# Kernel optimization log

Measured on AMD Instinct MI355X. Metric: run time of the kernel, lower is better.

Reference implementation:

```python
import jax, jax.numpy as jnp
import numpy as np

D = 256      # d_model
NH = 8       # heads
HD = D // NH # head dim = 32
NL = 4       # feature levels
NP = 4       # sampling points per head per level
DFF = 1024   # ffn hidden
LAYERS = 6
SHAPES = [(48, 48), (24, 24), (12, 12), (6, 6)]


def setup_inputs() -> dict:
    key = jax.random.key(0)
    ks = jax.random.split(key, 20)
    bs = 2
    inp = {}
    for i, (h, w) in enumerate(SHAPES):
        inp[f"src{i}"] = jax.random.normal(ks[i], (bs, D, h, w), jnp.float32)
        inp[f"pos{i}"] = jax.random.normal(ks[4 + i], (bs, D, h, w), jnp.float32)

    def p(k, shape, s=0.02):
        return jax.random.normal(k, shape, jnp.float32) * s

    inp["level_embed"] = p(ks[8], (NL, D), 1.0)
    inp["Wv"] = p(ks[9], (LAYERS, D, D))
    inp["bv"] = jnp.zeros((LAYERS, D))
    inp["Woff"] = p(ks[10], (LAYERS, D, NH * NL * NP * 2), 0.001)
    inp["boff"] = p(ks[11], (LAYERS, NH * NL * NP * 2), 0.5)
    inp["Wa"] = p(ks[12], (LAYERS, D, NH * NL * NP))
    inp["ba"] = jnp.zeros((LAYERS, NH * NL * NP))
    inp["Wo"] = p(ks[13], (LAYERS, D, D))
    inp["bo"] = jnp.zeros((LAYERS, D))
    inp["g1"] = jnp.ones((LAYERS, D))
    inp["beta1"] = jnp.zeros((LAYERS, D))
    inp["W1"] = p(ks[14], (LAYERS, D, DFF))
    inp["bf1"] = jnp.zeros((LAYERS, DFF))
    inp["W2"] = p(ks[15], (LAYERS, DFF, D))
    inp["bf2"] = jnp.zeros((LAYERS, D))
    inp["g2"] = jnp.ones((LAYERS, D))
    inp["beta2"] = jnp.zeros((LAYERS, D))
    return inp


def _ln(x, g, b):
    m = x.mean(-1, keepdims=True)
    v = ((x - m) ** 2).mean(-1, keepdims=True)
    return (x - m) / jnp.sqrt(v + 1e-5) * g + b


def _bilinear(value, loc, H, W):
    # value: (bs, NH, H*W, HD); loc: (bs, Len, NH, NP, 2) in [0,1]
    # grid_sample, align_corners=False, zero padding
    bs, Len, nh, P, _ = loc.shape
    x = loc[..., 0] * W - 0.5
    y = loc[..., 1] * H - 0.5
    x0 = jnp.floor(x)
    y0 = jnp.floor(y)
    lx = x - x0
    ly = y - y0
    x0i = x0.astype(jnp.int32)
    y0i = y0.astype(jnp.int32)
    out = jnp.zeros((bs, nh, Len, P, value.shape[-1]), value.dtype)
    for dy, dx, w in ((0, 0, (1 - lx) * (1 - ly)), (0, 1, lx * (1 - ly)),
                      (1, 0, (1 - lx) * ly), (1, 1, lx * ly)):
        xi = x0i + dx
        yi = y0i + dy
        valid = (xi >= 0) & (xi < W) & (yi >= 0) & (yi < H)
        idx = jnp.clip(yi, 0, H - 1) * W + jnp.clip(xi, 0, W - 1)  # (bs,Len,NH,P)
        idx_t = idx.transpose(0, 2, 1, 3).reshape(bs, nh, Len * P)
        v = jnp.take_along_axis(value, idx_t[..., None], axis=2)
        v = v.reshape(bs, nh, Len, P, -1)
        wm = (w * valid).transpose(0, 2, 1, 3)  # (bs,NH,Len,P)
        out = out + v * wm[..., None]
    return out


def _msda(q, src, ref, shapes, starts, Wv, bv, Woff, boff, Wa, ba, Wo, bo):
    bs, Len, _ = q.shape
    value = (src @ Wv + bv).reshape(bs, Len, NH, HD)
    off = (q @ Woff + boff).reshape(bs, Len, NH, NL, NP, 2)
    attn = jax.nn.softmax((q @ Wa + ba).reshape(bs, Len, NH, NL * NP), -1)
    attn = attn.reshape(bs, Len, NH, NL, NP)
    acc = jnp.zeros((bs, NH, Len, HD), q.dtype)
    for lv, (H, W) in enumerate(shapes):
        norm = jnp.array([W, H], q.dtype)
        loc = ref[None, :, None, None, :] + off[:, :, :, lv] / norm  # (bs,Len,NH,NP,2)
        v = value[:, starts[lv]:starts[lv] + H * W].transpose(0, 2, 1, 3)
        samp = _bilinear(v, loc, H, W)  # (bs,NH,Len,NP,HD)
        acc = acc + (samp * attn[:, :, :, lv].transpose(0, 2, 1, 3)[..., None]).sum(3)
    return acc.transpose(0, 2, 1, 3).reshape(bs, Len, D) @ Wo + bo


def _encode(srcs, poss, level_embed, Wv, bv, Woff, boff, Wa, ba, Wo, bo,
            g1, beta1, W1, bf1, W2, bf2, g2, beta2):
    shapes = [(s.shape[2], s.shape[3]) for s in srcs]
    bs = srcs[0].shape[0]
    src_flat = jnp.concatenate(
        [s.reshape(bs, D, -1).transpose(0, 2, 1) for s in srcs], 1)
    pos_flat = jnp.concatenate(
        [p.reshape(bs, D, -1).transpose(0, 2, 1) + level_embed[i][None, None]
         for i, p in enumerate(poss)], 1)
    starts = np.cumsum([0] + [h * w for h, w in shapes])[:-1]
    # reference points (masks are all-zero so valid_ratios == 1)
    refs = []
    for (H, W) in shapes:
        ry, rx = jnp.meshgrid(jnp.linspace(0.5, H - 0.5, H) / H,
                              jnp.linspace(0.5, W - 0.5, W) / W, indexing='ij')
        refs.append(jnp.stack([rx.reshape(-1), ry.reshape(-1)], -1))
    ref = jnp.concatenate(refs, 0)  # (Len, 2)

    out = src_flat
    for l in range(LAYERS):
        q = out + pos_flat
        out2 = _msda(q, out, ref, shapes, starts, Wv[l], bv[l], Woff[l],
                     boff[l], Wa[l], ba[l], Wo[l], bo[l])
        out = _ln(out + out2, g1[l], beta1[l])
        h = jax.nn.relu(out @ W1[l] + bf1[l])
        out = _ln(out + h @ W2[l] + bf2[l], g2[l], beta2[l])
    return out, shapes, starts


def reference(src0, src1, src2, src3, pos0, pos1, pos2, pos3, level_embed,
              Wv, bv, Woff, boff, Wa, ba, Wo, bo,
              g1, beta1, W1, bf1, W2, bf2, g2, beta2):
    memory, shapes, starts = _encode(
        [src0, src1, src2, src3], [pos0, pos1, pos2, pos3], level_embed,
        Wv, bv, Woff, boff, Wa, ba, Wo, bo,
        g1, beta1, W1, bf1, W2, bf2, g2, beta2)
    spatial_shapes = jnp.array(shapes, jnp.int32)
    level_start_index = jnp.array(np.asarray(starts), jnp.int32)
    return memory, spatial_shapes, level_start_index
```

## Files before the change

kernel.cpp:

```cpp
#include <hip/hip_runtime.h>
#include <math.h>

#define D_MODEL 256
#define NHEAD 8
#define HDIM 32
#define NLVL 4
#define NPTS 4
#define DFF 1024
#define NLAYERS 6
#define LEN 3060
#define BS 2
#define MROWS (BS * LEN)
#define MPAD 6144

typedef __attribute__((ext_vector_type(8))) short bf16x8;
typedef __attribute__((ext_vector_type(4))) float f32x4;

__device__ __forceinline__ unsigned short f2bf(float f) {
    union { float f; unsigned u; } v; v.f = f;
    unsigned r = v.u + 0x7FFF + ((v.u >> 16) & 1);
    return (unsigned short)(r >> 16);
}

#define GLDS(gp, lp) __builtin_amdgcn_global_load_lds(                        \
    (const __attribute__((address_space(1))) void*)(gp),                      \
    (__attribute__((address_space(3))) void*)(lp), 16, 0, 0)

__global__ __launch_bounds__(256) void flatten_kernel(
    const float* __restrict__ s0, const float* __restrict__ s1,
    const float* __restrict__ s2, const float* __restrict__ s3,
    const float* __restrict__ p0, const float* __restrict__ p1,
    const float* __restrict__ p2, const float* __restrict__ p3,
    const float* __restrict__ lemb,
    float* __restrict__ out, unsigned short* __restrict__ outbf,
    float* __restrict__ pos)
{
    int gid = blockIdx.x * 256 + threadIdx.x;
    if (gid >= MROWS * D_MODEL) return;
    int d  = gid & (D_MODEL - 1);
    int bt = gid >> 8;
    int b  = (bt >= LEN) ? 1 : 0;
    int t  = bt - b * LEN;

    int lv, li, hw;
    const float* sp; const float* pp;
    if (t < 2304)      { lv = 0; li = t;        hw = 2304; sp = s0; pp = p0; }
    else if (t < 2880) { lv = 1; li = t - 2304; hw = 576;  sp = s1; pp = p1; }
    else if (t < 3024) { lv = 2; li = t - 2880; hw = 144;  sp = s2; pp = p2; }
    else               { lv = 3; li = t - 3024; hw = 36;   sp = s3; pp = p3; }

    size_t si = (size_t)(b * D_MODEL + d) * hw + li;
    float v = sp[si];
    out[gid]   = v;
    outbf[gid] = f2bf(v);
    pos[gid]   = pp[si] + lemb[lv * D_MODEL + d];
}

__global__ __launch_bounds__(256) void addq_kernel(
    const float4* __restrict__ a, const float4* __restrict__ b,
    ushort4* __restrict__ qbf, int n4)
{
    int i = blockIdx.x * 256 + threadIdx.x;
    if (i >= n4) return;
    float4 x = a[i], y = b[i];
    qbf[i] = make_ushort4(f2bf(x.x + y.x), f2bf(x.y + y.y),
                          f2bf(x.z + y.z), f2bf(x.w + y.w));
}

__global__ __launch_bounds__(256) void wconv_kernel(
    const float* __restrict__ Wv, const float* __restrict__ Woff,
    const float* __restrict__ Wa, const float* __restrict__ Wo,
    const float* __restrict__ W1, const float* __restrict__ W2,
    unsigned short* __restrict__ Wv_t, unsigned short* __restrict__ Woffa_t,
    unsigned short* __restrict__ Wo_t, unsigned short* __restrict__ W1_t,
    unsigned short* __restrict__ W2_t)
{
    __shared__ float tile[32][33];
    int bid = blockIdx.x;
    int layer = bid / 736, r = bid % 736;
    const float* src; unsigned short* dst;
    int N, tk, tn, dstRowOff = 0, dstLd;
    if (r < 64)       { src = Wv  + layer*65536;  dst = Wv_t   + layer*65536;  N = 256;  int t2 = r;       tk = t2 >> 3; tn = t2 & 7;  dstLd = 256;  }
    else if (r < 128) { src = Woff+ layer*65536;  dst = Woffa_t+ layer*98304;  N = 256;  int t2 = r - 64;  tk = t2 >> 3; tn = t2 & 7;  dstLd = 256;  }
    else if (r < 160) { src = Wa  + layer*32768;  dst = Woffa_t+ layer*98304;  N = 128;  int t2 = r - 128; tk = t2 >> 2; tn = t2 & 3;  dstLd = 256;  dstRowOff = 256; }
    else if (r < 224) { src = Wo  + layer*65536;  dst = Wo_t   + layer*65536;  N = 256;  int t2 = r - 160; tk = t2 >> 3; tn = t2 & 7;  dstLd = 256;  }
    else if (r < 480) { src = W1  + layer*262144; dst = W1_t   + layer*262144; N = 1024; int t2 = r - 224; tk = t2 >> 5; tn = t2 & 31; dstLd = 256;  }
    else              { src = W2  + layer*262144; dst = W2_t   + layer*262144; N = 256;  int t2 = r - 480; tk = t2 >> 3; tn = t2 & 7;  dstLd = 1024; }
    int k0 = tk * 32, n0 = tn * 32;
    int tx = threadIdx.x & 31, ty = threadIdx.x >> 5;
    #pragma unroll
    for (int i = 0; i < 4; ++i)
        tile[ty + i*8][tx] = src[(size_t)(k0 + ty + i*8) * N + n0 + tx];
    __syncthreads();
    #pragma unroll
    for (int i = 0; i < 4; ++i)
        dst[(size_t)(dstRowOff + n0 + ty + i*8) * dstLd + k0 + tx] =
            f2bf(tile[tx][ty + i*8]);
}

template<bool RELU, bool OUTBF>
__global__ __launch_bounds__(256) void mfma_gemm(
    const unsigned short* __restrict__ A, const unsigned short* __restrict__ Bt,
    const float* __restrict__ bias, const float* __restrict__ bias2, int split,
    void* __restrict__ Cout, int M, int N, int K)
{
    __shared__ __align__(16) unsigned short lds[6144];
    const int tid  = threadIdx.x;
    const int lane = tid & 63, wave = tid >> 6;
    const int wm = wave >> 1, wn = wave & 1;
    const int row0 = blockIdx.y * 128, col0 = blockIdx.x * 64;
    const int l15 = lane & 15, l4 = lane >> 4;
    char* ldsb = (char*)lds;

    const unsigned short* aSrc[2]; char* aDst[2];
    #pragma unroll
    for (int i = 0; i < 2; ++i) {
        int u = i*256 + wave*64 + lane;
        int rr = u >> 2, kb = u & 3, kbd = kb ^ (rr & 3);
        aSrc[i] = A + (size_t)(row0 + rr) * K + kbd * 8;
        aDst[i] = ldsb + (i*256 + wave*64) * 16;
    }
    const unsigned short* bSrc; char* bDst;
    {
        int u = tid, cc = u >> 2, kb = u & 3, kbd = kb ^ (cc & 3);
        bSrc = Bt + (size_t)(col0 + cc) * K + kbd * 8;
        bDst = ldsb + 8192 + wave * 1024;
    }

    int a_off[4], b_off[2];
    #pragma unroll
    for (int mf = 0; mf < 4; ++mf) {
        int rr = wm*64 + mf*16 + l15;
        a_off[mf] = rr*64 + ((l4 ^ (rr & 3)) << 4);
    }
    #pragma unroll
    for (int nf = 0; nf < 2; ++nf) {
        int cc = wn*32 + nf*16 + l15;
        b_off[nf] = 8192 + cc*64 + ((l4 ^ (cc & 3)) << 4);
    }

    f32x4 acc[4][2];
    #pragma unroll
    for (int mf = 0; mf < 4; ++mf)
        #pragma unroll
        for (int nf = 0; nf < 2; ++nf)
            acc[mf][nf] = (f32x4)(0.f);

    for (int k0 = 0; k0 < K; k0 += 32) {
        GLDS(aSrc[0] + k0, aDst[0]);
        GLDS(aSrc[1] + k0, aDst[1]);
        GLDS(bSrc    + k0, bDst);
        __syncthreads();
        bf16x8 bfr[2];
        #pragma unroll
        for (int nf = 0; nf < 2; ++nf)
            bfr[nf] = *(const bf16x8*)(ldsb + b_off[nf]);
        #pragma unroll
        for (int mf = 0; mf < 4; ++mf) {
            bf16x8 afr = *(const bf16x8*)(ldsb + a_off[mf]);
            #pragma unroll
            for (int nf = 0; nf < 2; ++nf)
                acc[mf][nf] = __builtin_amdgcn_mfma_f32_16x16x32_bf16(
                    afr, bfr[nf], acc[mf][nf], 0, 0, 0);
        }
        __syncthreads();
    }

    #pragma unroll
    for (int nf = 0; nf < 2; ++nf) {
        int col = col0 + wn*32 + nf*16 + l15;
        float bb = (col < split) ? bias[col] : bias2[col - split];
        #pragma unroll
        for (int mf = 0; mf < 4; ++mf) {
            #pragma unroll
            for (int i = 0; i < 4; ++i) {
                int row = row0 + wm*64 + mf*16 + l4*4 + i;
                if (row < M) {
                    float v = acc[mf][nf][i] + bb;
                    if (RELU) v = fmaxf(v, 0.f);
                    if (OUTBF)
                        ((unsigned short*)Cout)[(size_t)row * N + col] = f2bf(v);
                    else
                        ((float*)Cout)[(size_t)row * N + col] = v;
                }
            }
        }
    }
}

__global__ __launch_bounds__(256) void msda_kernel(
    const float* __restrict__ value,
    const float* __restrict__ offattn,
    unsigned short* __restrict__ outb)
{
    int gid = blockIdx.x * 256 + threadIdx.x;
    if (gid >= MROWS * NHEAD * 8) return;
    int part = gid & 7;
    int h    = (gid >> 3) & 7;
    int bt   = gid >> 6;
    int b    = (bt >= LEN) ? 1 : 0;
    int t    = bt - b * LEN;

    const float* lg = offattn + (size_t)bt * 384 + 256 + h * 16;
    float w[16];
    float mx = -1e30f;
    #pragma unroll
    for (int j = 0; j < 16; ++j) { w[j] = lg[j]; mx = fmaxf(mx, w[j]); }
    float s = 0.f;
    #pragma unroll
    for (int j = 0; j < 16; ++j) { w[j] = __expf(w[j] - mx); s += w[j]; }
    float inv = 1.f / s;

    int li, Wr;
    if (t < 2304)      { li = t;        Wr = 48; }
    else if (t < 2880) { li = t - 2304; Wr = 24; }
    else if (t < 3024) { li = t - 2880; Wr = 12; }
    else               { li = t - 3024; Wr = 6;  }
    float refx = ((li % Wr) + 0.5f) / (float)Wr;
    float refy = ((li / Wr) + 0.5f) / (float)Wr;

    const float* offp    = offattn + (size_t)bt * 384 + h * 32;
    const float* valbase = value + (size_t)b * LEN * D_MODEL + h * HDIM + part * 4;

    const int starts[4] = {0, 2304, 2880, 3024};
    const int Ws[4]     = {48, 24, 12, 6};

    float4 acc = make_float4(0.f, 0.f, 0.f, 0.f);

    #pragma unroll
    for (int lv = 0; lv < NLVL; ++lv) {
        int Wl = Ws[lv];
        int st = starts[lv];
        float fW = (float)Wl;
        #pragma unroll
        for (int p = 0; p < NPTS; ++p) {
            float ox = offp[(lv * NPTS + p) * 2 + 0];
            float oy = offp[(lv * NPTS + p) * 2 + 1];
            float x = (refx + ox / fW) * fW - 0.5f;
            float y = (refy + oy / fW) * fW - 0.5f;
            float x0f = floorf(x), y0f = floorf(y);
            float lx = x - x0f, ly = y - y0f;
            int x0 = (int)x0f, y0 = (int)y0f;
            float aw = w[lv * NPTS + p] * inv;
            float tw[4] = {(1.f - lx) * (1.f - ly), lx * (1.f - ly),
                           (1.f - lx) * ly,         lx * ly};
            const int dxs[4] = {0, 1, 0, 1};
            const int dys[4] = {0, 0, 1, 1};
            #pragma unroll
            for (int tap = 0; tap < 4; ++tap) {
                int xi = x0 + dxs[tap], yi = y0 + dys[tap];
                bool valid = (xi >= 0) & (xi < Wl) & (yi >= 0) & (yi < Wl);
                int xc = xi < 0 ? 0 : (xi > Wl - 1 ? Wl - 1 : xi);
                int yc = yi < 0 ? 0 : (yi > Wl - 1 ? Wl - 1 : yi);
                int tt = st + yc * Wl + xc;
                const float4 v = *(const float4*)(valbase + (size_t)tt * D_MODEL);
                float wt = valid ? aw * tw[tap] : 0.f;
                acc.x += wt * v.x; acc.y += wt * v.y;
                acc.z += wt * v.z; acc.w += wt * v.w;
            }
        }
    }
    ushort4 o = make_ushort4(f2bf(acc.x), f2bf(acc.y), f2bf(acc.z), f2bf(acc.w));
    *(ushort4*)(outb + (size_t)bt * D_MODEL + h * HDIM + part * 4) = o;
}

__global__ __launch_bounds__(256) void add_ln_kernel(
    float* __restrict__ out, unsigned short* __restrict__ outbf,
    const float* __restrict__ add,
    const float* __restrict__ g, const float* __restrict__ be)
{
    int row  = blockIdx.x * 4 + (threadIdx.x >> 6);
    int lane = threadIdx.x & 63;
    if (row >= MROWS) return;

    float4 x = ((const float4*)(out + (size_t)row * D_MODEL))[lane];
    float4 y = ((const float4*)(add + (size_t)row * D_MODEL))[lane];
    x.x += y.x; x.y += y.y; x.z += y.z; x.w += y.w;

    float s  = x.x + x.y + x.z + x.w;
    float ss = x.x * x.x + x.y * x.y + x.z * x.z + x.w * x.w;
    #pragma unroll
    for (int m = 1; m < 64; m <<= 1) {
        s  += __shfl_xor(s, m);
        ss += __shfl_xor(ss, m);
    }
    float mean = s * (1.f / 256.f);
    float var  = ss * (1.f / 256.f) - mean * mean;
    float rstd = rsqrtf(var + 1e-5f);

    float4 gv = ((const float4*)g)[lane];
    float4 bv = ((const float4*)be)[lane];
    float4 o;
    o.x = (x.x - mean) * rstd * gv.x + bv.x;
    o.y = (x.y - mean) * rstd * gv.y + bv.y;
    o.z = (x.z - mean) * rstd * gv.z + bv.z;
    o.w = (x.w - mean) * rstd * gv.w + bv.w;
    ((float4*)(out + (size_t)row * D_MODEL))[lane] = o;
    ((ushort4*)(outbf + (size_t)row * D_MODEL))[lane] =
        make_ushort4(f2bf(o.x), f2bf(o.y), f2bf(o.z), f2bf(o.w));
}

__global__ void tail_kernel(float* __restrict__ tail)
{
    if (threadIdx.x == 0 && blockIdx.x == 0) {
        const float vals[12] = {48.f, 48.f, 24.f, 24.f, 12.f, 12.f, 6.f, 6.f,
                                0.f, 2304.f, 2880.f, 3024.f};
        #pragma unroll
        for (int i = 0; i < 12; ++i) tail[i] = vals[i];
    }
}

extern "C" void kernel_launch(void* const* d_in, const int* in_sizes, int n_in,
                              void* d_out, int out_size, void* d_ws, size_t ws_size,
                              hipStream_t stream)
{
    const float* SRC[4]; const float* POS[4];
    bool interleaved = (in_sizes[1] == in_sizes[0]);
    if (interleaved) {
        SRC[0] = (const float*)d_in[0]; POS[0] = (const float*)d_in[1];
        SRC[1] = (const float*)d_in[2]; POS[1] = (const float*)d_in[3];
        SRC[2] = (const float*)d_in[4]; POS[2] = (const float*)d_in[5];
        SRC[3] = (const float*)d_in[6]; POS[3] = (const float*)d_in[7];
    } else {
        for (int i = 0; i < 4; ++i) {
            SRC[i] = (const float*)d_in[i];
            POS[i] = (const float*)d_in[4 + i];
        }
    }
    const float* lemb  = (const float*)d_in[8];
    const float* Wv    = (const float*)d_in[9];
    const float* bv    = (const float*)d_in[10];
    const float* Woff  = (const float*)d_in[11];
    const float* boff  = (const float*)d_in[12];
    const float* Wa    = (const float*)d_in[13];
    const float* ba    = (const float*)d_in[14];
    const float* Wo    = (const float*)d_in[15];
    const float* bo    = (const float*)d_in[16];
    const float* g1    = (const float*)d_in[17];
    const float* beta1 = (const float*)d_in[18];
    const float* W1    = (const float*)d_in[19];
    const float* bf1   = (const float*)d_in[20];
    const float* W2    = (const float*)d_in[21];
    const float* bf2   = (const float*)d_in[22];
    const float* g2    = (const float*)d_in[23];
    const float* beta2 = (const float*)d_in[24];

    float* out = (float*)d_out;

    char* ws = (char*)d_ws;
    float* pos     = (float*)ws;                                   ws += (size_t)MPAD * 256 * 4;
    float* val     = (float*)ws;                                   ws += (size_t)MPAD * 256 * 4;
    float* offattn = (float*)ws;                                   ws += (size_t)MPAD * 384 * 4;
    float* tmp     = (float*)ws;                                   ws += (size_t)MPAD * 256 * 4;
    unsigned short* qbf    = (unsigned short*)ws;                  ws += (size_t)MPAD * 256 * 2;
    unsigned short* outbf  = (unsigned short*)ws;                  ws += (size_t)MPAD * 256 * 2;
    unsigned short* msdabf = (unsigned short*)ws;                  ws += (size_t)MPAD * 256 * 2;
    unsigned short* hbuf   = (unsigned short*)ws;                  ws += (size_t)MPAD * 1024 * 2;
    unsigned short* Wv_t    = (unsigned short*)ws;                 ws += (size_t)6 * 65536 * 2;
    unsigned short* Woffa_t = (unsigned short*)ws;                 ws += (size_t)6 * 98304 * 2;
    unsigned short* Wo_t    = (unsigned short*)ws;                 ws += (size_t)6 * 65536 * 2;
    unsigned short* W1_t    = (unsigned short*)ws;                 ws += (size_t)6 * 262144 * 2;
    unsigned short* W2_t    = (unsigned short*)ws;                 ws += (size_t)6 * 262144 * 2;

    wconv_kernel<<<6 * 736, 256, 0, stream>>>(Wv, Woff, Wa, Wo, W1, W2,
                                              Wv_t, Woffa_t, Wo_t, W1_t, W2_t);

    const int nElem = MROWS * D_MODEL;
    flatten_kernel<<<(nElem + 255) / 256, 256, 0, stream>>>(
        SRC[0], SRC[1], SRC[2], SRC[3], POS[0], POS[1], POS[2], POS[3],
        lemb, out, outbf, pos);

    const int n4 = nElem / 4;
    const dim3 g256(256 / 64, MPAD / 128);
    const dim3 g384(384 / 64, MPAD / 128);
    const dim3 g1024(1024 / 64, MPAD / 128);

    for (int l = 0; l < NLAYERS; ++l) {
        const unsigned short* Wv_l   = Wv_t    + (size_t)l * 65536;
        const unsigned short* Woffa_l= Woffa_t + (size_t)l * 98304;
        const unsigned short* Wo_l   = Wo_t    + (size_t)l * 65536;
        const unsigned short* W1_l   = W1_t    + (size_t)l * 262144;
        const unsigned short* W2_l   = W2_t    + (size_t)l * 262144;
        const float* bv_l  = bv   + l * 256;
        const float* boff_l= boff + l * 256;
        const float* ba_l  = ba   + l * 128;
        const float* bo_l  = bo   + l * 256;
        const float* bf1_l = bf1  + l * DFF;
        const float* bf2_l = bf2  + l * 256;

        addq_kernel<<<(n4 + 255) / 256, 256, 0, stream>>>(
            (const float4*)out, (const float4*)pos, (ushort4*)qbf, n4);

        mfma_gemm<false, false><<<g256, 256, 0, stream>>>(
            outbf, Wv_l, bv_l, bv_l, 256, val, MROWS, 256, 256);

        mfma_gemm<false, false><<<g384, 256, 0, stream>>>(
            qbf, Woffa_l, boff_l, ba_l, 256, offattn, MROWS, 384, 256);

        msda_kernel<<<(MROWS * NHEAD * 8 + 255) / 256, 256, 0, stream>>>(
            val, offattn, msdabf);

        mfma_gemm<false, false><<<g256, 256, 0, stream>>>(
            msdabf, Wo_l, bo_l, bo_l, 256, tmp, MROWS, 256, 256);

        add_ln_kernel<<<MROWS / 4, 256, 0, stream>>>(
            out, outbf, tmp, g1 + l * 256, beta1 + l * 256);

        mfma_gemm<true, true><<<g1024, 256, 0, stream>>>(
            outbf, W1_l, bf1_l, bf1_l, 1024, hbuf, MROWS, 1024, 256);

        mfma_gemm<false, false><<<g256, 256, 0, stream>>>(
            hbuf, W2_l, bf2_l, bf2_l, 256, tmp, MROWS, 256, 1024);

        add_ln_kernel<<<MROWS / 4, 256, 0, stream>>>(
            out, outbf, tmp, g2 + l * 256, beta2 + l * 256);
    }

    tail_kernel<<<1, 64, 0, stream>>>(out + (size_t)MROWS * D_MODEL);
}
```

Baseline: 744.0 us.

## Double-buffer GEMM K=64 tiles, fuse value/offset GEMMs, bf16 value, fold q-add into LN

The GEMM core now stages 64-wide K tiles in double-buffered LDS with a new layout and prefetches the next tile while computing the current one. The value and offset/attention projections run as one launch, and the value tensor is stored in bf16 so the sampling kernel gathers half the bytes. The separate q = out + pos kernel is removed: flatten and the second layer norm now emit the bf16 query directly. This trades fewer launches and less memory traffic for more LDS per block (lower occupancy) and extra rounding of the value tensor.

```diff
diff --git a/kernel.cpp b/kernel.cpp
--- a/kernel.cpp
+++ b/kernel.cpp
@@ -21,6 +21,10 @@
     unsigned r = v.u + 0x7FFF + ((v.u >> 16) & 1);
     return (unsigned short)(r >> 16);
 }
+__device__ __forceinline__ float bf2f(unsigned short s) {
+    union { unsigned u; float f; } v; v.u = ((unsigned)s) << 16;
+    return v.f;
+}
 
 #define GLDS(gp, lp) __builtin_amdgcn_global_load_lds(                        \
     (const __attribute__((address_space(1))) void*)(gp),                      \
@@ -33,7 +37,7 @@
     const float* __restrict__ p2, const float* __restrict__ p3,
     const float* __restrict__ lemb,
     float* __restrict__ out, unsigned short* __restrict__ outbf,
-    float* __restrict__ pos)
+    unsigned short* __restrict__ qbf, float* __restrict__ pos)
 {
     int gid = blockIdx.x * 256 + threadIdx.x;
     if (gid >= MROWS * D_MODEL) return;
@@ -51,20 +55,11 @@
 
     size_t si = (size_t)(b * D_MODEL + d) * hw + li;
     float v = sp[si];
+    float pv = pp[si] + lemb[lv * D_MODEL + d];
     out[gid]   = v;
     outbf[gid] = f2bf(v);
-    pos[gid]   = pp[si] + lemb[lv * D_MODEL + d];
-}
-
-__global__ __launch_bounds__(256) void addq_kernel(
-    const float4* __restrict__ a, const float4* __restrict__ b,
-    ushort4* __restrict__ qbf, int n4)
-{
-    int i = blockIdx.x * 256 + threadIdx.x;
-    if (i >= n4) return;
-    float4 x = a[i], y = b[i];
-    qbf[i] = make_ushort4(f2bf(x.x + y.x), f2bf(x.y + y.y),
-                          f2bf(x.z + y.z), f2bf(x.w + y.w));
+    qbf[gid]   = f2bf(v + pv);
+    pos[gid]   = pv;
 }
 
 __global__ __launch_bounds__(256) void wconv_kernel(
@@ -98,84 +93,101 @@
             f2bf(tile[tx][ty + i*8]);
 }
 
-template<bool RELU, bool OUTBF>
-__global__ __launch_bounds__(256) void mfma_gemm(
+__device__ __forceinline__ void gemm_core(
     const unsigned short* __restrict__ A, const unsigned short* __restrict__ Bt,
-    const float* __restrict__ bias, const float* __restrict__ bias2, int split,
-    void* __restrict__ Cout, int M, int N, int K)
-{
-    __shared__ __align__(16) unsigned short lds[6144];
+    int row0, int col0, int K, char* smem, f32x4 (&acc)[4][2])
+{
     const int tid  = threadIdx.x;
     const int lane = tid & 63, wave = tid >> 6;
     const int wm = wave >> 1, wn = wave & 1;
-    const int row0 = blockIdx.y * 128, col0 = blockIdx.x * 64;
     const int l15 = lane & 15, l4 = lane >> 4;
-    char* ldsb = (char*)lds;
-
-    const unsigned short* aSrc[2]; char* aDst[2];
+
+    const unsigned short* aS[4]; const unsigned short* bS[2];
+    int aD[4], bD[2];
+    #pragma unroll
+    for (int i = 0; i < 4; ++i) {
+        int c = i*256 + tid, q = c >> 7, r = c & 127;
+        aS[i] = A + (size_t)(row0 + r) * K + q*8;
+        aD[i] = c * 16;
+    }
     #pragma unroll
     for (int i = 0; i < 2; ++i) {
-        int u = i*256 + wave*64 + lane;
-        int rr = u >> 2, kb = u & 3, kbd = kb ^ (rr & 3);
-        aSrc[i] = A + (size_t)(row0 + rr) * K + kbd * 8;
-        aDst[i] = ldsb + (i*256 + wave*64) * 16;
-    }
-    const unsigned short* bSrc; char* bDst;
-    {
-        int u = tid, cc = u >> 2, kb = u & 3, kbd = kb ^ (cc & 3);
-        bSrc = Bt + (size_t)(col0 + cc) * K + kbd * 8;
-        bDst = ldsb + 8192 + wave * 1024;
-    }
-
-    int a_off[4], b_off[2];
-    #pragma unroll
-    for (int mf = 0; mf < 4; ++mf) {
-        int rr = wm*64 + mf*16 + l15;
-        a_off[mf] = rr*64 + ((l4 ^ (rr & 3)) << 4);
-    }
-    #pragma unroll
-    for (int nf = 0; nf < 2; ++nf) {
-        int cc = wn*32 + nf*16 + l15;
-        b_off[nf] = 8192 + cc*64 + ((l4 ^ (cc & 3)) << 4);
-    }
-
-    f32x4 acc[4][2];
+        int c = i*256 + tid, q = c >> 6, n = c & 63;
+        bS[i] = Bt + (size_t)(col0 + n) * K + q*8;
+        bD[i] = 16384 + c * 16;
+    }
+
+    int aOff[4][2], bOff[2][2];
     #pragma unroll
     for (int mf = 0; mf < 4; ++mf)
         #pragma unroll
-        for (int nf = 0; nf < 2; ++nf)
-            acc[mf][nf] = (f32x4)(0.f);
-
-    for (int k0 = 0; k0 < K; k0 += 32) {
-        GLDS(aSrc[0] + k0, aDst[0]);
-        GLDS(aSrc[1] + k0, aDst[1]);
-        GLDS(bSrc    + k0, bDst);
-        __syncthreads();
-        bf16x8 bfr[2];
-        #pragma unroll
-        for (int nf = 0; nf < 2; ++nf)
-            bfr[nf] = *(const bf16x8*)(ldsb + b_off[nf]);
-        #pragma unroll
-        for (int mf = 0; mf < 4; ++mf) {
-            bf16x8 afr = *(const bf16x8*)(ldsb + a_off[mf]);
+        for (int s = 0; s < 2; ++s)
+            aOff[mf][s] = ((s*4 + l4)*128 + wm*64 + mf*16 + l15) * 16;
+    #pragma unroll
+    for (int nf = 0; nf < 2; ++nf)
+        #pragma unroll
+        for (int s = 0; s < 2; ++s)
+            bOff[nf][s] = 16384 + ((s*4 + l4)*64 + wn*32 + nf*16 + l15) * 16;
+
+    #pragma unroll
+    for (int i = 0; i < 4; ++i) GLDS(aS[i], smem + aD[i]);
+    #pragma unroll
+    for (int i = 0; i < 2; ++i) GLDS(bS[i], smem + bD[i]);
+    __syncthreads();
+
+    const int nt = K >> 6;
+    for (int t = 0; t < nt; ++t) {
+        const int bo = (t & 1) * 24576;
+        if (t + 1 < nt) {
+            const int nbo = ((t + 1) & 1) * 24576;
+            const int k0 = (t + 1) << 6;
+            #pragma unroll
+            for (int i = 0; i < 4; ++i) GLDS(aS[i] + k0, smem + nbo + aD[i]);
+            #pragma unroll
+            for (int i = 0; i < 2; ++i) GLDS(bS[i] + k0, smem + nbo + bD[i]);
+        }
+        #pragma unroll
+        for (int s = 0; s < 2; ++s) {
+            bf16x8 bfr[2];
             #pragma unroll
             for (int nf = 0; nf < 2; ++nf)
-                acc[mf][nf] = __builtin_amdgcn_mfma_f32_16x16x32_bf16(
-                    afr, bfr[nf], acc[mf][nf], 0, 0, 0);
+                bfr[nf] = *(const bf16x8*)(smem + bo + bOff[nf][s]);
+            #pragma unroll
+            for (int mf = 0; mf < 4; ++mf) {
+                bf16x8 afr = *(const bf16x8*)(smem + bo + aOff[mf][s]);
+                #pragma unroll
+                for (int nf = 0; nf < 2; ++nf)
+                    acc[mf][nf] = __builtin_amdgcn_mfma_f32_16x16x32_bf16(
+                        afr, bfr[nf], acc[mf][nf], 0, 0, 0);
+            }
         }
         __syncthreads();
     }
-
+}
+
+template<bool RELU, bool OUTBF>
+__global__ __launch_bounds__(256) void gemm3(
+    const unsigned short* __restrict__ A, const unsigned short* __restrict__ Bt,
+    const float* __restrict__ bias, void* __restrict__ Cout, int N, int K)
+{
+    __shared__ __align__(16) char smem[49152];
+    f32x4 acc[4][2] = {};
+    const int row0 = blockIdx.y * 128, col0 = blockIdx.x * 64;
+    gemm_core(A, Bt, row0, col0, K, smem, acc);
+
+    const int lane = threadIdx.x & 63, wave = threadIdx.x >> 6;
+    const int wm = wave >> 1, wn = wave & 1;
+    const int l15 = lane & 15, l4 = lane >> 4;
     #pragma unroll
     for (int nf = 0; nf < 2; ++nf) {
         int col = col0 + wn*32 + nf*16 + l15;
-        float bb = (col < split) ? bias[col] : bias2[col - split];
-        #pragma unroll
-        for (int mf = 0; mf < 4; ++mf) {
+        float bb = bias[col];
+        #pragma unroll
+        for (int mf = 0; mf < 4; ++mf)
             #pragma unroll
             for (int i = 0; i < 4; ++i) {
                 int row = row0 + wm*64 + mf*16 + l4*4 + i;
-                if (row < M) {
+                if (row < MROWS) {
                     float v = acc[mf][nf][i] + bb;
                     if (RELU) v = fmaxf(v, 0.f);
                     if (OUTBF)
@@ -184,12 +196,52 @@
                         ((float*)Cout)[(size_t)row * N + col] = v;
                 }
             }
-        }
+    }
+}
+
+__global__ __launch_bounds__(256) void gemm_va(
+    const unsigned short* __restrict__ outbf, const unsigned short* __restrict__ qbf,
+    const unsigned short* __restrict__ Wv_l, const unsigned short* __restrict__ Woffa_l,
+    const float* __restrict__ bv, const float* __restrict__ boff,
+    const float* __restrict__ ba,
+    unsigned short* __restrict__ valbf, float* __restrict__ offattn)
+{
+    __shared__ __align__(16) char smem[49152];
+    const int bx = blockIdx.x;
+    const bool isV = bx < 4;
+    const unsigned short* A  = isV ? outbf : qbf;
+    const unsigned short* Bt = isV ? Wv_l : Woffa_l;
+    const int col0 = isV ? bx * 64 : (bx - 4) * 64;
+    const int row0 = blockIdx.y * 128;
+
+    f32x4 acc[4][2] = {};
+    gemm_core(A, Bt, row0, col0, 256, smem, acc);
+
+    const int lane = threadIdx.x & 63, wave = threadIdx.x >> 6;
+    const int wm = wave >> 1, wn = wave & 1;
+    const int l15 = lane & 15, l4 = lane >> 4;
+    #pragma unroll
+    for (int nf = 0; nf < 2; ++nf) {
+        int col = col0 + wn*32 + nf*16 + l15;
+        float bb = isV ? bv[col] : (col < 256 ? boff[col] : ba[col - 256]);
+        #pragma unroll
+        for (int mf = 0; mf < 4; ++mf)
+            #pragma unroll
+            for (int i = 0; i < 4; ++i) {
+                int row = row0 + wm*64 + mf*16 + l4*4 + i;
+                if (row < MROWS) {
+                    float v = acc[mf][nf][i] + bb;
+                    if (isV)
+                        valbf[(size_t)row * 256 + col] = f2bf(v);
+                    else
+                        offattn[(size_t)row * 384 + col] = v;
+                }
+            }
     }
 }
 
 __global__ __launch_bounds__(256) void msda_kernel(
-    const float* __restrict__ value,
+    const unsigned short* __restrict__ value,
     const float* __restrict__ offattn,
     unsigned short* __restrict__ outb)
 {
@@ -219,8 +271,9 @@
     float refx = ((li % Wr) + 0.5f) / (float)Wr;
     float refy = ((li / Wr) + 0.5f) / (float)Wr;
 
-    const float* offp    = offattn + (size_t)bt * 384 + h * 32;
-    const float* valbase = value + (size_t)b * LEN * D_MODEL + h * HDIM + part * 4;
+    const float* offp = offattn + (size_t)bt * 384 + h * 32;
+    const unsigned short* valbase =
+        value + (size_t)b * LEN * D_MODEL + h * HDIM + part * 4;
 
     const int starts[4] = {0, 2304, 2880, 3024};
     const int Ws[4]     = {48, 24, 12, 6};
@@ -230,7 +283,7 @@
     #pragma unroll
     for (int lv = 0; lv < NLVL; ++lv) {
         int Wl = Ws[lv];
-        int st = starts[lv];
+        int stt = starts[lv];
         float fW = (float)Wl;
         #pragma unroll
         for (int p = 0; p < NPTS; ++p) {
@@ -252,11 +305,11 @@
                 bool valid = (xi >= 0) & (xi < Wl) & (yi >= 0) & (yi < Wl);
                 int xc = xi < 0 ? 0 : (xi > Wl - 1 ? Wl - 1 : xi);
                 int yc = yi < 0 ? 0 : (yi > Wl - 1 ? Wl - 1 : yi);
-                int tt = st + yc * Wl + xc;
-                const float4 v = *(const float4*)(valbase + (size_t)tt * D_MODEL);
+                int tt = stt + yc * Wl + xc;
+                ushort4 vv = *(const ushort4*)(valbase + (size_t)tt * D_MODEL);
                 float wt = valid ? aw * tw[tap] : 0.f;
-                acc.x += wt * v.x; acc.y += wt * v.y;
-                acc.z += wt * v.z; acc.w += wt * v.w;
+                acc.x += wt * bf2f(vv.x); acc.y += wt * bf2f(vv.y);
+                acc.z += wt * bf2f(vv.z); acc.w += wt * bf2f(vv.w);
             }
         }
     }
@@ -264,10 +317,12 @@
     *(ushort4*)(outb + (size_t)bt * D_MODEL + h * HDIM + part * 4) = o;
 }
 
+template<bool WITH_POS>
 __global__ __launch_bounds__(256) void add_ln_kernel(
     float* __restrict__ out, unsigned short* __restrict__ outbf,
     const float* __restrict__ add,
-    const float* __restrict__ g, const float* __restrict__ be)
+    const float* __restrict__ g, const float* __restrict__ be,
+    const float* __restrict__ pos, unsigned short* __restrict__ qbf)
 {
     int row  = blockIdx.x * 4 + (threadIdx.x >> 6);
     int lane = threadIdx.x & 63;
@@ -298,6 +353,12 @@
     ((float4*)(out + (size_t)row * D_MODEL))[lane] = o;
     ((ushort4*)(outbf + (size_t)row * D_MODEL))[lane] =
         make_ushort4(f2bf(o.x), f2bf(o.y), f2bf(o.z), f2bf(o.w));
+    if (WITH_POS) {
+        float4 pv = ((const float4*)(pos + (size_t)row * D_MODEL))[lane];
+        ((ushort4*)(qbf + (size_t)row * D_MODEL))[lane] =
+            make_ushort4(f2bf(o.x + pv.x), f2bf(o.y + pv.y),
+                         f2bf(o.z + pv.z), f2bf(o.w + pv.w));
+    }
 }
 
 __global__ void tail_kernel(float* __restrict__ tail)
@@ -348,19 +409,19 @@
     float* out = (float*)d_out;
 
     char* ws = (char*)d_ws;
-    float* pos     = (float*)ws;                                   ws += (size_t)MPAD * 256 * 4;
-    float* val     = (float*)ws;                                   ws += (size_t)MPAD * 256 * 4;
-    float* offattn = (float*)ws;                                   ws += (size_t)MPAD * 384 * 4;
-    float* tmp     = (float*)ws;                                   ws += (size_t)MPAD * 256 * 4;
-    unsigned short* qbf    = (unsigned short*)ws;                  ws += (size_t)MPAD * 256 * 2;
-    unsigned short* outbf  = (unsigned short*)ws;                  ws += (size_t)MPAD * 256 * 2;
-    unsigned short* msdabf = (unsigned short*)ws;                  ws += (size_t)MPAD * 256 * 2;
-    unsigned short* hbuf   = (unsigned short*)ws;                  ws += (size_t)MPAD * 1024 * 2;
-    unsigned short* Wv_t    = (unsigned short*)ws;                 ws += (size_t)6 * 65536 * 2;
-    unsigned short* Woffa_t = (unsigned short*)ws;                 ws += (size_t)6 * 98304 * 2;
-    unsigned short* Wo_t    = (unsigned short*)ws;                 ws += (size_t)6 * 65536 * 2;
-    unsigned short* W1_t    = (unsigned short*)ws;                 ws += (size_t)6 * 262144 * 2;
-    unsigned short* W2_t    = (unsigned short*)ws;                 ws += (size_t)6 * 262144 * 2;
+    float* pos     = (float*)ws;                   ws += (size_t)MPAD * 256 * 4;
+    float* offattn = (float*)ws;                   ws += (size_t)MPAD * 384 * 4;
+    float* tmp     = (float*)ws;                   ws += (size_t)MPAD * 256 * 4;
+    unsigned short* qbf    = (unsigned short*)ws;  ws += (size_t)MPAD * 256 * 2;
+    unsigned short* outbf  = (unsigned short*)ws;  ws += (size_t)MPAD * 256 * 2;
+    unsigned short* msdabf = (unsigned short*)ws;  ws += (size_t)MPAD * 256 * 2;
+    unsigned short* valbf  = (unsigned short*)ws;  ws += (size_t)MPAD * 256 * 2;
+    unsigned short* hbuf   = (unsigned short*)ws;  ws += (size_t)MPAD * 1024 * 2;
+    unsigned short* Wv_t    = (unsigned short*)ws; ws += (size_t)6 * 65536 * 2;
+    unsigned short* Woffa_t = (unsigned short*)ws; ws += (size_t)6 * 98304 * 2;
+    unsigned short* Wo_t    = (unsigned short*)ws; ws += (size_t)6 * 65536 * 2;
+    unsigned short* W1_t    = (unsigned short*)ws; ws += (size_t)6 * 262144 * 2;
+    unsigned short* W2_t    = (unsigned short*)ws; ws += (size_t)6 * 262144 * 2;
 
     wconv_kernel<<<6 * 736, 256, 0, stream>>>(Wv, Woff, Wa, Wo, W1, W2,
                                               Wv_t, Woffa_t, Wo_t, W1_t, W2_t);
@@ -368,52 +429,41 @@
     const int nElem = MROWS * D_MODEL;
     flatten_kernel<<<(nElem + 255) / 256, 256, 0, stream>>>(
         SRC[0], SRC[1], SRC[2], SRC[3], POS[0], POS[1], POS[2], POS[3],
-        lemb, out, outbf, pos);
-
-    const int n4 = nElem / 4;
-    const dim3 g256(256 / 64, MPAD / 128);
-    const dim3 g384(384 / 64, MPAD / 128);
-    const dim3 g1024(1024 / 64, MPAD / 128);
+        lemb, out, outbf, qbf, pos);
+
+    const dim3 gVA(10, MPAD / 128);
+    const dim3 g256(4, MPAD / 128);
+    const dim3 g1024(16, MPAD / 128);
+    const int gLN = MROWS / 4;
 
     for (int l = 0; l < NLAYERS; ++l) {
-        const unsigned short* Wv_l   = Wv_t    + (size_t)l * 65536;
-        const unsigned short* Woffa_l= Woffa_t + (size_t)l * 98304;
-        const unsigned short* Wo_l   = Wo_t    + (size_t)l * 65536;
-        const unsigned short* W1_l   = W1_t    + (size_t)l * 262144;
-        const unsigned short* W2_l   = W2_t    + (size_t)l * 262144;
-        const float* bv_l  = bv   + l * 256;
-        const float* boff_l= boff + l * 256;
-        const float* ba_l  = ba   + l * 128;
-        const float* bo_l  = bo   + l * 256;
-        const float* bf1_l = bf1  + l * DFF;
-        const float* bf2_l = bf2  + l * 256;
-
-        addq_kernel<<<(n4 + 255) / 256, 256, 0, stream>>>(
-            (const float4*)out, (const float4*)pos, (ushort4*)qbf, n4);
-
-        mfma_gemm<false, false><<<g256, 256, 0, stream>>>(
-            outbf, Wv_l, bv_l, bv_l, 256, val, MROWS, 256, 256);
-
-        mfma_gemm<false, false><<<g384, 256, 0, stream>>>(
-            qbf, Woffa_l, boff_l, ba_l, 256, offattn, MROWS, 384, 256);
+        const unsigned short* Wv_l    = Wv_t    + (size_t)l * 65536;
+        const unsigned short* Woffa_l = Woffa_t + (size_t)l * 98304;
+        const unsigned short* Wo_l    = Wo_t    + (size_t)l * 65536;
+        const unsigned short* W1_l    = W1_t    + (size_t)l * 262144;
+        const unsigned short* W2_l    = W2_t    + (size_t)l * 262144;
+
+        gemm_va<<<gVA, 256, 0, stream>>>(
+            outbf, qbf, Wv_l, Woffa_l, bv + l * 256, boff + l * 256,
+            ba + l * 128, valbf, offattn);
 
         msda_kernel<<<(MROWS * NHEAD * 8 + 255) / 256, 256, 0, stream>>>(
-            val, offattn, msdabf);
-
-        mfma_gemm<false, false><<<g256, 256, 0, stream>>>(
-            msdabf, Wo_l, bo_l, bo_l, 256, tmp, MROWS, 256, 256);
-
-        add_ln_kernel<<<MROWS / 4, 256, 0, stream>>>(
-            out, outbf, tmp, g1 + l * 256, beta1 + l * 256);
-
-        mfma_gemm<true, true><<<g1024, 256, 0, stream>>>(
-            outbf, W1_l, bf1_l, bf1_l, 1024, hbuf, MROWS, 1024, 256);
-
-        mfma_gemm<false, false><<<g256, 256, 0, stream>>>(
-            hbuf, W2_l, bf2_l, bf2_l, 256, tmp, MROWS, 256, 1024);
-
-        add_ln_kernel<<<MROWS / 4, 256, 0, stream>>>(
-            out, outbf, tmp, g2 + l * 256, beta2 + l * 256);
+            valbf, offattn, msdabf);
+
+        gemm3<false, false><<<g256, 256, 0, stream>>>(
+            msdabf, Wo_l, bo + l * 256, tmp, 256, 256);
+
+        add_ln_kernel<false><<<gLN, 256, 0, stream>>>(
+            out, outbf, tmp, g1 + l * 256, beta1 + l * 256, pos, qbf);
+
+        gemm3<true, true><<<g1024, 256, 0, stream>>>(
+            outbf, W1_l, bf1 + l * DFF, hbuf, 1024, 256);
+
+        gemm3<false, false><<<g256, 256, 0, stream>>>(
+            hbuf, W2_l, bf2 + l * 256, tmp, 256, 1024);
+
+        add_ln_kernel<true><<<gLN, 256, 0, stream>>>(
+            out, outbf, tmp, g2 + l * 256, beta2 + l * 256, pos, qbf);
     }
 
     tail_kernel<<<1, 64, 0, stream>>>(out + (size_t)MROWS * D_MODEL);
```

Result: no change. 731.8 us (-1.6%).
